# Kernel tuning notes

Hardware: AMD Instinct MI355X
Metric: run time of the kernel (lower is better)

The kernel has to match this reference:

```python
import jax, jax.numpy as jnp
import numpy as np

B, S, IN, H, T, OUT = 128, 336, 64, 1024, 96, 1


def _lstm_step(h, c, x, W_ih, W_hh, b_ih, b_hh):
    # PyTorch LSTM cell: gates in (i, f, g, o) order
    g = x @ W_ih.T + b_ih + h @ W_hh.T + b_hh  # [B, 4H]
    i, f, gg, o = jnp.split(g, 4, axis=-1)
    c_new = jax.nn.sigmoid(f) * c + jax.nn.sigmoid(i) * jnp.tanh(gg)
    h_new = jax.nn.sigmoid(o) * jnp.tanh(c_new)
    return h_new, c_new


def setup_inputs() -> dict:
    key = jax.random.key(0)
    ks = jax.random.split(key, 12)
    s = 0.05
    return {
        "src": jax.random.normal(ks[0], (B, S, IN), jnp.float32),
        "enc_W_ih": jax.random.normal(ks[1], (4 * H, IN), jnp.float32) * s,
        "enc_W_hh": jax.random.normal(ks[2], (4 * H, H), jnp.float32) * s,
        "enc_b_ih": jax.random.normal(ks[3], (4 * H,), jnp.float32) * s,
        "enc_b_hh": jax.random.normal(ks[4], (4 * H,), jnp.float32) * s,
        "dec_W_ih": jax.random.normal(ks[5], (4 * H, OUT + H), jnp.float32) * s,
        "dec_W_hh": jax.random.normal(ks[6], (4 * H, H), jnp.float32) * s,
        "dec_b_ih": jax.random.normal(ks[7], (4 * H,), jnp.float32) * s,
        "dec_b_hh": jax.random.normal(ks[8], (4 * H,), jnp.float32) * s,
        "attn_W": jax.random.normal(ks[9], (H, H), jnp.float32) * s,
        "fc_W": jax.random.normal(ks[10], (OUT, H), jnp.float32) * s,
        "fc_b": jax.random.normal(ks[11], (OUT,), jnp.float32) * s,
        "target_len": T,
    }


def reference(src, enc_W_ih, enc_W_hh, enc_b_ih, enc_b_hh,
              dec_W_ih, dec_W_hh, dec_b_ih, dec_b_hh,
              attn_W, fc_W, fc_b, target_len):
    batch = src.shape[0]
    hdim = enc_W_hh.shape[1]

    # ---- Encoder: single-layer LSTM over src, batch_first ----
    def enc_step(carry, x_t):
        h, c = carry
        h, c = _lstm_step(h, c, x_t, enc_W_ih, enc_W_hh, enc_b_ih, enc_b_hh)
        return (h, c), h

    h0 = jnp.zeros((batch, hdim), src.dtype)
    c0 = jnp.zeros((batch, hdim), src.dtype)
    (h_enc, c_enc), enc_hs = jax.lax.scan(enc_step, (h0, c0),
                                          jnp.swapaxes(src, 0, 1))
    encoder_outputs = jnp.swapaxes(enc_hs, 0, 1)  # [B, S, H]

    def dec_step(carry, _):
        h, c, prev_y = carry
        q = h @ attn_W.T                                      # [B, H]
        energy = jnp.einsum('bh,bsh->bs', q, encoder_outputs)  # [B, S]
        w = jax.nn.softmax(energy, axis=-1)
        ctx = jnp.einsum('bs,bsh->bh', w, encoder_outputs)     # [B, H]
        x = jnp.concatenate([prev_y, ctx], axis=-1)            # [B, OUT+H]
        h, c = _lstm_step(h, c, x, dec_W_ih, dec_W_hh, dec_b_ih, dec_b_hh)
        pred = h @ fc_W.T + fc_b                               # [B, OUT]
        prev_y = jax.lax.stop_gradient(pred)                   # pred.detach()
        return (h, c, prev_y), pred

    prev_y0 = jnp.zeros((batch, fc_W.shape[0]), src.dtype)
    _, preds = jax.lax.scan(dec_step, (h_enc, c_enc, prev_y0), None,
                            length=target_len)
    return jnp.swapaxes(preds, 0, 1)  # [B, target_len, OUT]
```

## Files before the change

### kernel.cpp

```cpp
#include <hip/hip_runtime.h>
#include <math.h>

#define Bn   128
#define Sn   336
#define INd  64
#define Hn   1024
#define Tn   96
#define G4   4096
#define KCE  34
#define KCD  65
#define KCQ  32

typedef __attribute__((ext_vector_type(8))) short short8;
typedef __attribute__((ext_vector_type(4))) float floatx4;
typedef __attribute__((ext_vector_type(4))) unsigned int uintx4;

__device__ __forceinline__ float sigmoidf_(float x){ return 1.0f/(1.0f+expf(-x)); }

__device__ __forceinline__ unsigned short f2bf(float f){
    union { float f; unsigned u; } v; v.f = f;
    unsigned r = v.u + 0x7fffu + ((v.u >> 16) & 1u);
    return (unsigned short)(r >> 16);
}
__device__ __forceinline__ float bflo(unsigned u){ union{unsigned u; float f;} v; v.u = u << 16;        return v.f; }
__device__ __forceinline__ float bfhi(unsigned u){ union{unsigned u; float f;} v; v.u = u & 0xffff0000u; return v.f; }
__device__ __forceinline__ void unpack8v(uintx4 v, float* f){
    f[0]=bflo(v.x); f[1]=bfhi(v.x); f[2]=bflo(v.y); f[3]=bfhi(v.y);
    f[4]=bflo(v.z); f[5]=bfhi(v.z); f[6]=bflo(v.w); f[7]=bfhi(v.w);
}

__global__ void pack_encf(const float* __restrict__ Wih, const float* __restrict__ Whh,
                          const float* __restrict__ bih, const float* __restrict__ bhh,
                          unsigned short* __restrict__ Wp, float* __restrict__ bc){
    long n = (long)256*KCE*512;
    for (long idx = (long)blockIdx.x*256 + threadIdx.x; idx < n; idx += (long)gridDim.x*256){
        int j = (int)(idx & 7), l = (int)((idx >> 3) & 63);
        int kc = (int)((idx >> 9) % KCE);
        int s  = (int)(idx / (KCE*512));
        int c = l & 15, kg = l >> 4;
        int k = kc*32 + kg*8 + j;
        int gate = s & 3, unit = (s >> 2)*16 + c;
        int orig = gate*Hn + unit;
        float v = (k < INd) ? Wih[orig*INd + k] : Whh[(size_t)orig*Hn + (k - INd)];
        Wp[idx] = f2bf(v);
    }
    int tid = blockIdx.x*256 + threadIdx.x;
    if (tid < G4){
        int g = (tid >> 4) & 3, u = (tid >> 6)*16 + (tid & 15);
        int orig = g*Hn + u;
        bc[tid] = bih[orig] + bhh[orig];
    }
}

__global__ void pack_decf(const float* __restrict__ Wih, const float* __restrict__ Whh,
                          const float* __restrict__ bih, const float* __restrict__ bhh,
                          unsigned short* __restrict__ Wp, float* __restrict__ bc){
    long n = (long)256*KCD*512;
    for (long idx = (long)blockIdx.x*256 + threadIdx.x; idx < n; idx += (long)gridDim.x*256){
        int j = (int)(idx & 7), l = (int)((idx >> 3) & 63);
        int kc = (int)((idx >> 9) % KCD);
        int s  = (int)(idx / (KCD*512));
        int c = l & 15, kg = l >> 4;
        int k = kc*32 + kg*8 + j;
        int gate = s & 3, unit = (s >> 2)*16 + c;
        int orig = gate*Hn + unit;
        float v;
        if (k < Hn)          v = Wih[(size_t)orig*(Hn+1) + 1 + k];
        else if (k < 2*Hn)   v = Whh[(size_t)orig*Hn + (k - Hn)];
        else if (k == 2*Hn)  v = Wih[(size_t)orig*(Hn+1)];
        else                 v = 0.0f;
        Wp[idx] = f2bf(v);
    }
    int tid = blockIdx.x*256 + threadIdx.x;
    if (tid < G4){
        int g = (tid >> 4) & 3, u = (tid >> 6)*16 + (tid & 15);
        int orig = g*Hn + u;
        bc[tid] = bih[orig] + bhh[orig];
    }
}

__global__ void pack_attnf(const float* __restrict__ w, unsigned short* __restrict__ Wp){
    int n = 64*KCQ*512;
    for (int idx = blockIdx.x*256 + threadIdx.x; idx < n; idx += gridDim.x*256){
        int j = idx & 7, l = (idx >> 3) & 63;
        int kc = (idx >> 9) & 31;
        int s  = idx >> 14;
        int nn = s*16 + (l & 15);
        int k = kc*32 + (l >> 4)*8 + j;
        Wp[idx] = f2bf(w[(size_t)nn*Hn + k]);
    }
}

__global__ void conv_srcf(const float* __restrict__ s, unsigned short* __restrict__ d){
    int n = Sn*8*2*512;
    for (int idx = blockIdx.x*256 + threadIdx.x; idx < n; idx += gridDim.x*256){
        int j = idx & 7, l = (idx >> 3) & 63;
        int kc = (idx >> 9) & 1, rg = (idx >> 10) & 7, t = idx >> 13;
        int b = rg*16 + (l & 15);
        int k = kc*32 + (l >> 4)*8 + j;
        d[idx] = f2bf(s[((size_t)b*Sn + t)*INd + k]);
    }
}

__global__ void init_ws(unsigned short* __restrict__ hf0, float* __restrict__ cbuf,
                        unsigned short* __restrict__ A0, unsigned short* __restrict__ A1){
    for (int i = blockIdx.x*256 + threadIdx.x; i < 8*KCD*512; i += gridDim.x*256){
        A0[i] = 0; A1[i] = 0;
        if (i < 8*32*512) hf0[i] = 0;
        if (i < Bn*Hn) cbuf[i] = 0.0f;
    }
}

__device__ __forceinline__ void swz(int b, int& x, int& y){
    int xcd = b & 7, li = b >> 3;
    y = xcd*8 + (li & 7);
    x = li >> 3;
}

__global__ __launch_bounds__(256)
void enc_step(const unsigned short* __restrict__ srcfrag,
              const unsigned short* __restrict__ hin,
              const unsigned short* __restrict__ Wf,
              const float* __restrict__ bc, float* __restrict__ cbuf,
              unsigned short* __restrict__ hout,
              unsigned short* __restrict__ enco,
              unsigned short* __restrict__ adec0,
              int t, int last)
{
    __shared__ float red[2][16][65];
    const int tid = threadIdx.x, l = tid & 63, w = tid >> 6;
    const int rgw = w & 1, kh = w >> 1;
    int x, y; swz(blockIdx.x, x, y);
    const int rg = x*2 + rgw;
    const int m0 = rg*16;
    const unsigned short* Bf = Wf + (size_t)(4*y)*KCE*512 + l*8;
    const unsigned short* Ax = srcfrag + ((size_t)t*8 + rg)*2*512 + l*8;
    const unsigned short* Ah = hin + (size_t)rg*32*512 + l*8;
    floatx4 acc0={0,0,0,0}, acc1={0,0,0,0}, acc2={0,0,0,0}, acc3={0,0,0,0};

    if (kh == 0){
        #pragma unroll
        for (int kc = 0; kc < 2; kc++){
            short8 a  = *(const short8*)(Ax + kc*512);
            short8 b0 = *(const short8*)(Bf + (0*KCE + kc)*512);
            short8 b1 = *(const short8*)(Bf + (1*KCE + kc)*512);
            short8 b2 = *(const short8*)(Bf + (2*KCE + kc)*512);
            short8 b3 = *(const short8*)(Bf + (3*KCE + kc)*512);
            acc0 = __builtin_amdgcn_mfma_f32_16x16x32_bf16(a, b0, acc0, 0, 0, 0);
            acc1 = __builtin_amdgcn_mfma_f32_16x16x32_bf16(a, b1, acc1, 0, 0, 0);
            acc2 = __builtin_amdgcn_mfma_f32_16x16x32_bf16(a, b2, acc2, 0, 0, 0);
            acc3 = __builtin_amdgcn_mfma_f32_16x16x32_bf16(a, b3, acc3, 0, 0, 0);
        }
        #pragma unroll 5
        for (int hc = 0; hc < 15; hc++){
            short8 a  = *(const short8*)(Ah + hc*512);
            short8 b0 = *(const short8*)(Bf + (0*KCE + hc + 2)*512);
            short8 b1 = *(const short8*)(Bf + (1*KCE + hc + 2)*512);
            short8 b2 = *(const short8*)(Bf + (2*KCE + hc + 2)*512);
            short8 b3 = *(const short8*)(Bf + (3*KCE + hc + 2)*512);
            acc0 = __builtin_amdgcn_mfma_f32_16x16x32_bf16(a, b0, acc0, 0, 0, 0);
            acc1 = __builtin_amdgcn_mfma_f32_16x16x32_bf16(a, b1, acc1, 0, 0, 0);
            acc2 = __builtin_amdgcn_mfma_f32_16x16x32_bf16(a, b2, acc2, 0, 0, 0);
            acc3 = __builtin_amdgcn_mfma_f32_16x16x32_bf16(a, b3, acc3, 0, 0, 0);
        }
    } else {
        #pragma unroll 5
        for (int hc = 15; hc < 32; hc++){
            short8 a  = *(const short8*)(Ah + hc*512);
            short8 b0 = *(const short8*)(Bf + (0*KCE + hc + 2)*512);
            short8 b1 = *(const short8*)(Bf + (1*KCE + hc + 2)*512);
            short8 b2 = *(const short8*)(Bf + (2*KCE + hc + 2)*512);
            short8 b3 = *(const short8*)(Bf + (3*KCE + hc + 2)*512);
            acc0 = __builtin_amdgcn_mfma_f32_16x16x32_bf16(a, b0, acc0, 0, 0, 0);
            acc1 = __builtin_amdgcn_mfma_f32_16x16x32_bf16(a, b1, acc1, 0, 0, 0);
            acc2 = __builtin_amdgcn_mfma_f32_16x16x32_bf16(a, b2, acc2, 0, 0, 0);
            acc3 = __builtin_amdgcn_mfma_f32_16x16x32_bf16(a, b3, acc3, 0, 0, 0);
        }
        #pragma unroll
        for (int r = 0; r < 4; r++){
            red[rgw][ 0 + r][l] = acc0[r];
            red[rgw][ 4 + r][l] = acc1[r];
            red[rgw][ 8 + r][l] = acc2[r];
            red[rgw][12 + r][l] = acc3[r];
        }
    }
    __syncthreads();
    if (kh != 0) return;
    #pragma unroll
    for (int r = 0; r < 4; r++){
        acc0[r] += red[rgw][ 0 + r][l];
        acc1[r] += red[rgw][ 4 + r][l];
        acc2[r] += red[rgw][ 8 + r][l];
        acc3[r] += red[rgw][12 + r][l];
    }

    const int col = l & 15, q = l >> 4;
    const int u = y*16 + col;
    const float bi  = bc[y*64 + col];
    const float bf_ = bc[y*64 + 16 + col];
    const float bg  = bc[y*64 + 32 + col];
    const float bo  = bc[y*64 + 48 + col];
    const int lsh = ((u >> 3) & 3) * 16;
    #pragma unroll
    for (int r = 0; r < 4; r++){
        const int m = m0 + q*4 + r;
        float gi = acc0[r] + bi;
        float gf = acc1[r] + bf_;
        float gg = acc2[r] + bg;
        float go = acc3[r] + bo;
        float co = cbuf[(size_t)m*Hn + u];
        float cn = sigmoidf_(gf)*co + sigmoidf_(gi)*tanhf(gg);
        float hv = sigmoidf_(go)*tanhf(cn);
        cbuf[(size_t)m*Hn + u] = cn;
        unsigned short hb = f2bf(hv);
        const int lanep = (q*4 + r) + lsh;
        hout[(((size_t)rg*32 + (u >> 5))*64 + lanep)*8 + (u & 7)] = hb;
        __builtin_nontemporal_store(hb, enco + ((size_t)m*Sn + t)*Hn + u);
        if (last) adec0[(((size_t)rg*KCD + 32 + (u >> 5))*64 + lanep)*8 + (u & 7)] = hb;
    }
}

__global__ __launch_bounds__(256)
void dec_step(const unsigned short* __restrict__ Ac,
              const unsigned short* __restrict__ Wf,
              const float* __restrict__ bc, float* __restrict__ cbuf,
              unsigned short* __restrict__ An)
{
    __shared__ float red[2][16][65];
    const int tid = threadIdx.x, l = tid & 63, w = tid >> 6;
    const int rgw = w & 1, kh = w >> 1;
    int x, y; swz(blockIdx.x, x, y);
    const int rg = x*2 + rgw;
    const int m0 = rg*16;
    const unsigned short* Bf = Wf + (size_t)(4*y)*KCD*512 + l*8;
    const unsigned short* Af = Ac + (size_t)rg*KCD*512 + l*8;
    floatx4 acc0={0,0,0,0}, acc1={0,0,0,0}, acc2={0,0,0,0}, acc3={0,0,0,0};

    const int k0 = kh ? 33 : 0;
    const int k1 = kh ? KCD : 33;
    #pragma unroll 5
    for (int kc = k0; kc < k1; kc++){
        short8 a  = *(const short8*)(Af + kc*512);
        short8 b0 = *(const short8*)(Bf + (0*KCD + kc)*512);
        short8 b1 = *(const short8*)(Bf + (1*KCD + kc)*512);
        short8 b2 = *(const short8*)(Bf + (2*KCD + kc)*512);
        short8 b3 = *(const short8*)(Bf + (3*KCD + kc)*512);
        acc0 = __builtin_amdgcn_mfma_f32_16x16x32_bf16(a, b0, acc0, 0, 0, 0);
        acc1 = __builtin_amdgcn_mfma_f32_16x16x32_bf16(a, b1, acc1, 0, 0, 0);
        acc2 = __builtin_amdgcn_mfma_f32_16x16x32_bf16(a, b2, acc2, 0, 0, 0);
        acc3 = __builtin_amdgcn_mfma_f32_16x16x32_bf16(a, b3, acc3, 0, 0, 0);
    }
    if (kh != 0){
        #pragma unroll
        for (int r = 0; r < 4; r++){
            red[rgw][ 0 + r][l] = acc0[r];
            red[rgw][ 4 + r][l] = acc1[r];
            red[rgw][ 8 + r][l] = acc2[r];
            red[rgw][12 + r][l] = acc3[r];
        }
    }
    __syncthreads();
    if (kh != 0) return;
    #pragma unroll
    for (int r = 0; r < 4; r++){
        acc0[r] += red[rgw][ 0 + r][l];
        acc1[r] += red[rgw][ 4 + r][l];
        acc2[r] += red[rgw][ 8 + r][l];
        acc3[r] += red[rgw][12 + r][l];
    }

    const int col = l & 15, q = l >> 4;
    const int u = y*16 + col;
    const float bi  = bc[y*64 + col];
    const float bf_ = bc[y*64 + 16 + col];
    const float bg  = bc[y*64 + 32 + col];
    const float bo  = bc[y*64 + 48 + col];
    const int lsh = ((u >> 3) & 3) * 16;
    #pragma unroll
    for (int r = 0; r < 4; r++){
        const int m = m0 + q*4 + r;
        float gi = acc0[r] + bi;
        float gf = acc1[r] + bf_;
        float gg = acc2[r] + bg;
        float go = acc3[r] + bo;
        float co = cbuf[(size_t)m*Hn + u];
        float cn = sigmoidf_(gf)*co + sigmoidf_(gi)*tanhf(gg);
        float hv = sigmoidf_(go)*tanhf(cn);
        cbuf[(size_t)m*Hn + u] = cn;
        const int lanep = (q*4 + r) + lsh;
        An[(((size_t)rg*KCD + 32 + (u >> 5))*64 + lanep)*8 + (u & 7)] = f2bf(hv);
    }
}

__global__ __launch_bounds__(256)
void attnq_step(const unsigned short* __restrict__ Ac, const unsigned short* __restrict__ Wf,
                unsigned short* __restrict__ qout)
{
    __shared__ float red[2][4][65];
    const int tid = threadIdx.x, l = tid & 63, w = tid >> 6;
    const int rgw = w & 1, kh = w >> 1;
    int x, y; swz(blockIdx.x, x, y);
    const int rg = x*2 + rgw;
    const int m0 = rg*16;
    const unsigned short* Bf = Wf + (size_t)y*KCQ*512 + l*8;
    const unsigned short* Af = Ac + ((size_t)rg*KCD + 32)*512 + l*8;
    floatx4 acc = {0,0,0,0};
    const int k0 = kh ? 16 : 0;
    const int k1 = kh ? 32 : 16;
    #pragma unroll 8
    for (int kc = k0; kc < k1; kc++){
        short8 a = *(const short8*)(Af + kc*512);
        short8 b = *(const short8*)(Bf + kc*512);
        acc = __builtin_amdgcn_mfma_f32_16x16x32_bf16(a, b, acc, 0, 0, 0);
    }
    if (kh != 0){
        #pragma unroll
        for (int r = 0; r < 4; r++) red[rgw][r][l] = acc[r];
    }
    __syncthreads();
    if (kh != 0) return;
    #pragma unroll
    for (int r = 0; r < 4; r++) acc[r] += red[rgw][r][l];

    const int col = l & 15, q = l >> 4;
    #pragma unroll
    for (int r = 0; r < 4; r++){
        const int m = m0 + q*4 + r;
        qout[(size_t)m*Hn + y*16 + col] = f2bf(acc[r]);
    }
}

__global__ __launch_bounds__(512)
void fattn_kernel(const unsigned short* __restrict__ q,
                  const unsigned short* __restrict__ enc,
                  unsigned short* __restrict__ Ac,
                  const float* __restrict__ fcW, const float* __restrict__ fcb,
                  float* __restrict__ out, int d)
{
    __shared__ float ctxl[8*1024];
    __shared__ float mred[8], lred[8];
    __shared__ float fcred[128];
    const int b = blockIdx.x;
    const int tid = threadIdx.x, w = tid >> 6, l = tid & 63;

    float qv[16];
    {
        const uintx4* qp = (const uintx4*)(q + (size_t)b*Hn) + l*2;
        uintx4 q0 = qp[0], q1 = qp[1];
        unpack8v(q0, qv); unpack8v(q1, qv + 8);
    }
    float m = -1e30f, lsum = 0.0f;
    float cacc[16];
    #pragma unroll
    for (int i = 0; i < 16; i++) cacc[i] = 0.0f;

    const uintx4* ebase = (const uintx4*)(enc + (size_t)b*Sn*Hn) + l*2;
    for (int s = w; s < Sn; s += 8){
        uintx4 e0 = __builtin_nontemporal_load(ebase + (size_t)s*128);
        uintx4 e1 = __builtin_nontemporal_load(ebase + (size_t)s*128 + 1);
        float ev[16];
        unpack8v(e0, ev); unpack8v(e1, ev + 8);
        float part = 0.0f;
        #pragma unroll
        for (int i = 0; i < 16; i++) part = fmaf(qv[i], ev[i], part);
        #pragma unroll
        for (int off = 32; off; off >>= 1) part += __shfl_down(part, off);
        float e = __shfl(part, 0);
        float mn = fmaxf(m, e);
        float corr = expf(m - mn);
        float p = expf(e - mn);
        lsum = lsum*corr + p;
        if (corr != 1.0f){
            #pragma unroll
            for (int i = 0; i < 16; i++) cacc[i] *= corr;
        }
        #pragma unroll
        for (int i = 0; i < 16; i++) cacc[i] = fmaf(p, ev[i], cacc[i]);
        m = mn;
    }
    if (l == 0){ mred[w] = m; lred[w] = lsum; }
    __syncthreads();
    float M = mred[0];
    #pragma unroll
    for (int k = 1; k < 8; k++) M = fmaxf(M, mred[k]);
    float corr = expf(m - M);
    #pragma unroll
    for (int j = 0; j < 16; j++) ctxl[w*1024 + j*64 + l] = cacc[j]*corr;
    __syncthreads();
    float L = 0.0f;
    #pragma unroll
    for (int k = 0; k < 8; k++) L += lred[k]*expf(mred[k] - M);
    float invL = 1.0f / L;

    {
        const int u0 = 2*tid;
        float s0 = 0.0f, s1 = 0.0f;
        #pragma unroll
        for (int k = 0; k < 8; k++){
            s0 += ctxl[k*1024 + (u0 & 15)*64 + (u0 >> 4)];
            s1 += ctxl[k*1024 + ((u0+1) & 15)*64 + ((u0+1) >> 4)];
        }
        ushort2 cv; cv.x = f2bf(s0*invL); cv.y = f2bf(s1*invL);
        const int kc = u0 >> 5;
        const int lanep = (b & 15) + ((u0 >> 3) & 3)*16;
        *(ushort2*)(Ac + ((((size_t)(b >> 4))*KCD + kc)*64 + lanep)*8 + (u0 & 7)) = cv;
    }

    float part = 0.0f;
    if (tid < 128){
        const unsigned short* hp = Ac + ((((size_t)(b >> 4))*KCD + 32 + (tid >> 2))*64
                                         + (b & 15) + (tid & 3)*16)*8;
        uintx4 hv = *(const uintx4*)hp;
        float hf[8]; unpack8v(hv, hf);
        #pragma unroll
        for (int j = 0; j < 8; j++) part = fmaf(hf[j], fcW[tid*8 + j], part);
    }
    __syncthreads();
    if (tid < 128) fcred[tid] = part;
    __syncthreads();
    for (int o = 64; o; o >>= 1){
        if (tid < o && tid + o < 128) fcred[tid] += fcred[tid + o];
        __syncthreads();
    }
    if (tid == 0 && d > 0){
        float p = fcred[0] + fcb[0];
        out[b*Tn + (d - 1)] = p;
        Ac[(((size_t)(b >> 4))*KCD + 64)*512 + (b & 15)*8] = f2bf(p);
    }
}

__global__ __launch_bounds__(128)
void fc_final(const unsigned short* __restrict__ A, const float* __restrict__ fcW,
              const float* __restrict__ fcb, float* __restrict__ out){
    __shared__ float red[128];
    const int b = blockIdx.x, tid = threadIdx.x;
    const unsigned short* hp = A + ((((size_t)(b >> 4))*KCD + 32 + (tid >> 2))*64
                                     + (b & 15) + (tid & 3)*16)*8;
    uintx4 hv = *(const uintx4*)hp;
    float hf[8]; unpack8v(hv, hf);
    float part = 0.0f;
    #pragma unroll
    for (int j = 0; j < 8; j++) part = fmaf(hf[j], fcW[tid*8 + j], part);
    red[tid] = part; __syncthreads();
    for (int o = 64; o; o >>= 1){
        if (tid < o) red[tid] += red[tid + o];
        __syncthreads();
    }
    if (tid == 0) out[b*Tn + (Tn - 1)] = red[0] + fcb[0];
}

extern "C" void kernel_launch(void* const* d_in, const int* in_sizes, int n_in,
                              void* d_out, int out_size, void* d_ws, size_t ws_size,
                              hipStream_t stream){
    const float* src  = (const float*)d_in[0];
    const float* eWih = (const float*)d_in[1];
    const float* eWhh = (const float*)d_in[2];
    const float* ebih = (const float*)d_in[3];
    const float* ebhh = (const float*)d_in[4];
    const float* dWih = (const float*)d_in[5];
    const float* dWhh = (const float*)d_in[6];
    const float* dbih = (const float*)d_in[7];
    const float* dbhh = (const float*)d_in[8];
    const float* attnW= (const float*)d_in[9];
    const float* fcW  = (const float*)d_in[10];
    const float* fcb  = (const float*)d_in[11];
    float* out = (float*)d_out;

    char* base = (char*)d_ws;
    auto alloc = [&](size_t bytes){ void* p = base; base += (bytes + 255) & ~255ull; return p; };
    unsigned short* Wencf = (unsigned short*)alloc((size_t)256*KCE*512*2);
    float*          benc  = (float*)alloc(G4*4);
    unsigned short* Wdecf = (unsigned short*)alloc((size_t)256*KCD*512*2);
    float*          bdec  = (float*)alloc(G4*4);
    unsigned short* Wattf = (unsigned short*)alloc((size_t)64*KCQ*512*2);
    unsigned short* srcf  = (unsigned short*)alloc((size_t)Sn*8*2*512*2);
    unsigned short* enco  = (unsigned short*)alloc((size_t)Bn*Sn*Hn*2);
    unsigned short* hf0   = (unsigned short*)alloc((size_t)8*32*512*2);
    unsigned short* hf1   = (unsigned short*)alloc((size_t)8*32*512*2);
    float*          cbuf  = (float*)alloc((size_t)Bn*Hn*4);
    unsigned short* A0f   = (unsigned short*)alloc((size_t)8*KCD*512*2);
    unsigned short* A1f   = (unsigned short*)alloc((size_t)8*KCD*512*2);
    unsigned short* qbf   = (unsigned short*)alloc((size_t)Bn*Hn*2);

    conv_srcf<<<2048, 256, 0, stream>>>(src, srcf);
    pack_encf<<<4096, 256, 0, stream>>>(eWih, eWhh, ebih, ebhh, Wencf, benc);
    pack_decf<<<8192, 256, 0, stream>>>(dWih, dWhh, dbih, dbhh, Wdecf, bdec);
    pack_attnf<<<1024, 256, 0, stream>>>(attnW, Wattf);
    init_ws<<<1040, 256, 0, stream>>>(hf0, cbuf, A0f, A1f);

    unsigned short* hf[2] = {hf0, hf1};
    unsigned short* Ad[2] = {A0f, A1f};

    for (int t = 0; t < Sn; t++){
        enc_step<<<256, 256, 0, stream>>>(srcf, hf[t&1], Wencf, benc, cbuf,
                                          hf[(t+1)&1], enco, A0f, t, t == Sn-1);
    }
    for (int d = 0; d < Tn; d++){
        unsigned short* Ac = Ad[d&1];
        unsigned short* An = Ad[(d+1)&1];
        attnq_step<<<256, 256, 0, stream>>>(Ac, Wattf, qbf);
        fattn_kernel<<<Bn, 512, 0, stream>>>(qbf, enco, Ac, fcW, fcb, out, d);
        dec_step<<<256, 256, 0, stream>>>(Ac, Wdecf, bdec, cbuf, An);
    }
    fc_final<<<Bn, 128, 0, stream>>>(Ad[0], fcW, fcb, out);
}
```

Measured before the change: 9.487 ms.

## Fuse encoder timesteps into one persistent kernel with grid-wide flag barrier

```diff
diff --git a/kernel.cpp b/kernel.cpp
--- a/kernel.cpp
+++ b/kernel.cpp
@@ -103,11 +103,13 @@
 }
 
 __global__ void init_ws(unsigned short* __restrict__ hf0, float* __restrict__ cbuf,
-                        unsigned short* __restrict__ A0, unsigned short* __restrict__ A1){
+                        unsigned short* __restrict__ A0, unsigned short* __restrict__ A1,
+                        unsigned* __restrict__ bar){
     for (int i = blockIdx.x*256 + threadIdx.x; i < 8*KCD*512; i += gridDim.x*256){
         A0[i] = 0; A1[i] = 0;
         if (i < 8*32*512) hf0[i] = 0;
         if (i < Bn*Hn) cbuf[i] = 0.0f;
+        if (i < 256*16 + 16) bar[i] = 0;
     }
 }
 
@@ -117,15 +119,15 @@
     x = li >> 3;
 }
 
-__global__ __launch_bounds__(256)
-void enc_step(const unsigned short* __restrict__ srcfrag,
-              const unsigned short* __restrict__ hin,
-              const unsigned short* __restrict__ Wf,
-              const float* __restrict__ bc, float* __restrict__ cbuf,
-              unsigned short* __restrict__ hout,
-              unsigned short* __restrict__ enco,
-              unsigned short* __restrict__ adec0,
-              int t, int last)
+__global__ __launch_bounds__(256, 1)
+void enc_persist(const unsigned short* __restrict__ srcfrag,
+                 const unsigned short* __restrict__ Wf,
+                 const float* __restrict__ bc, float* __restrict__ cbuf,
+                 unsigned short* __restrict__ h0, unsigned short* __restrict__ h1,
+                 unsigned short* __restrict__ enco,
+                 unsigned short* __restrict__ adec0,
+                 unsigned* __restrict__ flags,
+                 unsigned* __restrict__ go)
 {
     __shared__ float red[2][16][65];
     const int tid = threadIdx.x, l = tid & 63, w = tid >> 6;
@@ -134,66 +136,6 @@
     const int rg = x*2 + rgw;
     const int m0 = rg*16;
     const unsigned short* Bf = Wf + (size_t)(4*y)*KCE*512 + l*8;
-    const unsigned short* Ax = srcfrag + ((size_t)t*8 + rg)*2*512 + l*8;
-    const unsigned short* Ah = hin + (size_t)rg*32*512 + l*8;
-    floatx4 acc0={0,0,0,0}, acc1={0,0,0,0}, acc2={0,0,0,0}, acc3={0,0,0,0};
-
-    if (kh == 0){
-        #pragma unroll
-        for (int kc = 0; kc < 2; kc++){
-            short8 a  = *(const short8*)(Ax + kc*512);
-            short8 b0 = *(const short8*)(Bf + (0*KCE + kc)*512);
-            short8 b1 = *(const short8*)(Bf + (1*KCE + kc)*512);
-            short8 b2 = *(const short8*)(Bf + (2*KCE + kc)*512);
-            short8 b3 = *(const short8*)(Bf + (3*KCE + kc)*512);
-            acc0 = __builtin_amdgcn_mfma_f32_16x16x32_bf16(a, b0, acc0, 0, 0, 0);
-            acc1 = __builtin_amdgcn_mfma_f32_16x16x32_bf16(a, b1, acc1, 0, 0, 0);
-            acc2 = __builtin_amdgcn_mfma_f32_16x16x32_bf16(a, b2, acc2, 0, 0, 0);
-            acc3 = __builtin_amdgcn_mfma_f32_16x16x32_bf16(a, b3, acc3, 0, 0, 0);
-        }
-        #pragma unroll 5
-        for (int hc = 0; hc < 15; hc++){
-            short8 a  = *(const short8*)(Ah + hc*512);
-            short8 b0 = *(const short8*)(Bf + (0*KCE + hc + 2)*512);
-            short8 b1 = *(const short8*)(Bf + (1*KCE + hc + 2)*512);
-            short8 b2 = *(const short8*)(Bf + (2*KCE + hc + 2)*512);
-            short8 b3 = *(const short8*)(Bf + (3*KCE + hc + 2)*512);
-            acc0 = __builtin_amdgcn_mfma_f32_16x16x32_bf16(a, b0, acc0, 0, 0, 0);
-            acc1 = __builtin_amdgcn_mfma_f32_16x16x32_bf16(a, b1, acc1, 0, 0, 0);
-            acc2 = __builtin_amdgcn_mfma_f32_16x16x32_bf16(a, b2, acc2, 0, 0, 0);
-            acc3 = __builtin_amdgcn_mfma_f32_16x16x32_bf16(a, b3, acc3, 0, 0, 0);
-        }
-    } else {
-        #pragma unroll 5
-        for (int hc = 15; hc < 32; hc++){
-            short8 a  = *(const short8*)(Ah + hc*512);
-            short8 b0 = *(const short8*)(Bf + (0*KCE + hc + 2)*512);
-            short8 b1 = *(const short8*)(Bf + (1*KCE + hc + 2)*512);
-            short8 b2 = *(const short8*)(Bf + (2*KCE + hc + 2)*512);
-            short8 b3 = *(const short8*)(Bf + (3*KCE + hc + 2)*512);
-            acc0 = __builtin_amdgcn_mfma_f32_16x16x32_bf16(a, b0, acc0, 0, 0, 0);
-            acc1 = __builtin_amdgcn_mfma_f32_16x16x32_bf16(a, b1, acc1, 0, 0, 0);
-            acc2 = __builtin_amdgcn_mfma_f32_16x16x32_bf16(a, b2, acc2, 0, 0, 0);
-            acc3 = __builtin_amdgcn_mfma_f32_16x16x32_bf16(a, b3, acc3, 0, 0, 0);
-        }
-        #pragma unroll
-        for (int r = 0; r < 4; r++){
-            red[rgw][ 0 + r][l] = acc0[r];
-            red[rgw][ 4 + r][l] = acc1[r];
-            red[rgw][ 8 + r][l] = acc2[r];
-            red[rgw][12 + r][l] = acc3[r];
-        }
-    }
-    __syncthreads();
-    if (kh != 0) return;
-    #pragma unroll
-    for (int r = 0; r < 4; r++){
-        acc0[r] += red[rgw][ 0 + r][l];
-        acc1[r] += red[rgw][ 4 + r][l];
-        acc2[r] += red[rgw][ 8 + r][l];
-        acc3[r] += red[rgw][12 + r][l];
-    }
-
     const int col = l & 15, q = l >> 4;
     const int u = y*16 + col;
     const float bi  = bc[y*64 + col];
@@ -201,22 +143,118 @@
     const float bg  = bc[y*64 + 32 + col];
     const float bo  = bc[y*64 + 48 + col];
     const int lsh = ((u >> 3) & 3) * 16;
-    #pragma unroll
-    for (int r = 0; r < 4; r++){
-        const int m = m0 + q*4 + r;
-        float gi = acc0[r] + bi;
-        float gf = acc1[r] + bf_;
-        float gg = acc2[r] + bg;
-        float go = acc3[r] + bo;
-        float co = cbuf[(size_t)m*Hn + u];
-        float cn = sigmoidf_(gf)*co + sigmoidf_(gi)*tanhf(gg);
-        float hv = sigmoidf_(go)*tanhf(cn);
-        cbuf[(size_t)m*Hn + u] = cn;
-        unsigned short hb = f2bf(hv);
-        const int lanep = (q*4 + r) + lsh;
-        hout[(((size_t)rg*32 + (u >> 5))*64 + lanep)*8 + (u & 7)] = hb;
-        __builtin_nontemporal_store(hb, enco + ((size_t)m*Sn + t)*Hn + u);
-        if (last) adec0[(((size_t)rg*KCD + 32 + (u >> 5))*64 + lanep)*8 + (u & 7)] = hb;
+    float creg[4] = {0,0,0,0};
+    unsigned short* hb[2] = {h0, h1};
+
+    for (int t = 0; t < Sn; t++){
+        const unsigned short* hin = hb[t & 1];
+        unsigned short* hout = hb[(t + 1) & 1];
+        const unsigned short* Ax = srcfrag + ((size_t)t*8 + rg)*2*512 + l*8;
+        const unsigned short* Ah = hin + (size_t)rg*32*512 + l*8;
+        floatx4 acc0={0,0,0,0}, acc1={0,0,0,0}, acc2={0,0,0,0}, acc3={0,0,0,0};
+
+        if (kh == 0){
+            #pragma unroll
+            for (int kc = 0; kc < 2; kc++){
+                short8 a  = *(const short8*)(Ax + kc*512);
+                short8 b0 = *(const short8*)(Bf + (0*KCE + kc)*512);
+                short8 b1 = *(const short8*)(Bf + (1*KCE + kc)*512);
+                short8 b2 = *(const short8*)(Bf + (2*KCE + kc)*512);
+                short8 b3 = *(const short8*)(Bf + (3*KCE + kc)*512);
+                acc0 = __builtin_amdgcn_mfma_f32_16x16x32_bf16(a, b0, acc0, 0, 0, 0);
+                acc1 = __builtin_amdgcn_mfma_f32_16x16x32_bf16(a, b1, acc1, 0, 0, 0);
+                acc2 = __builtin_amdgcn_mfma_f32_16x16x32_bf16(a, b2, acc2, 0, 0, 0);
+                acc3 = __builtin_amdgcn_mfma_f32_16x16x32_bf16(a, b3, acc3, 0, 0, 0);
+            }
+            #pragma unroll 5
+            for (int hc = 0; hc < 15; hc++){
+                short8 a  = *(const short8*)(Ah + hc*512);
+                short8 b0 = *(const short8*)(Bf + (0*KCE + hc + 2)*512);
+                short8 b1 = *(const short8*)(Bf + (1*KCE + hc + 2)*512);
+                short8 b2 = *(const short8*)(Bf + (2*KCE + hc + 2)*512);
+                short8 b3 = *(const short8*)(Bf + (3*KCE + hc + 2)*512);
+                acc0 = __builtin_amdgcn_mfma_f32_16x16x32_bf16(a, b0, acc0, 0, 0, 0);
+                acc1 = __builtin_amdgcn_mfma_f32_16x16x32_bf16(a, b1, acc1, 0, 0, 0);
+                acc2 = __builtin_amdgcn_mfma_f32_16x16x32_bf16(a, b2, acc2, 0, 0, 0);
+                acc3 = __builtin_amdgcn_mfma_f32_16x16x32_bf16(a, b3, acc3, 0, 0, 0);
+            }
+        } else {
+            #pragma unroll 5
+            for (int hc = 15; hc < 32; hc++){
+                short8 a  = *(const short8*)(Ah + hc*512);
+                short8 b0 = *(const short8*)(Bf + (0*KCE + hc + 2)*512);
+                short8 b1 = *(const short8*)(Bf + (1*KCE + hc + 2)*512);
+                short8 b2 = *(const short8*)(Bf + (2*KCE + hc + 2)*512);
+                short8 b3 = *(const short8*)(Bf + (3*KCE + hc + 2)*512);
+                acc0 = __builtin_amdgcn_mfma_f32_16x16x32_bf16(a, b0, acc0, 0, 0, 0);
+                acc1 = __builtin_amdgcn_mfma_f32_16x16x32_bf16(a, b1, acc1, 0, 0, 0);
+                acc2 = __builtin_amdgcn_mfma_f32_16x16x32_bf16(a, b2, acc2, 0, 0, 0);
+                acc3 = __builtin_amdgcn_mfma_f32_16x16x32_bf16(a, b3, acc3, 0, 0, 0);
+            }
+            #pragma unroll
+            for (int r = 0; r < 4; r++){
+                red[rgw][ 0 + r][l] = acc0[r];
+                red[rgw][ 4 + r][l] = acc1[r];
+                red[rgw][ 8 + r][l] = acc2[r];
+                red[rgw][12 + r][l] = acc3[r];
+            }
+        }
+        __syncthreads();
+        if (kh == 0){
+            #pragma unroll
+            for (int r = 0; r < 4; r++){
+                acc0[r] += red[rgw][ 0 + r][l];
+                acc1[r] += red[rgw][ 4 + r][l];
+                acc2[r] += red[rgw][ 8 + r][l];
+                acc3[r] += red[rgw][12 + r][l];
+            }
+            #pragma unroll
+            for (int r = 0; r < 4; r++){
+                const int m = m0 + q*4 + r;
+                float gi = acc0[r] + bi;
+                float gf = acc1[r] + bf_;
+                float gg = acc2[r] + bg;
+                float go_ = acc3[r] + bo;
+                float cn = sigmoidf_(gf)*creg[r] + sigmoidf_(gi)*tanhf(gg);
+                creg[r] = cn;
+                float hv = sigmoidf_(go_)*tanhf(cn);
+                unsigned short hbv = f2bf(hv);
+                const int lanep = (q*4 + r) + lsh;
+                hout[(((size_t)rg*32 + (u >> 5))*64 + lanep)*8 + (u & 7)] = hbv;
+                __builtin_nontemporal_store(hbv, enco + ((size_t)m*Sn + t)*Hn + u);
+                if (t == Sn - 1){
+                    adec0[(((size_t)rg*KCD + 32 + (u >> 5))*64 + lanep)*8 + (u & 7)] = hbv;
+                    cbuf[(size_t)m*Hn + u] = cn;
+                }
+            }
+        }
+        __syncthreads();
+        if (t == Sn - 1) break;
+
+        if (tid == 0)
+            __hip_atomic_store(flags + blockIdx.x*16, (unsigned)(t + 1),
+                               __ATOMIC_RELEASE, __HIP_MEMORY_SCOPE_AGENT);
+        if (blockIdx.x == 0){
+            if (tid < 64){
+                #pragma unroll
+                for (int g = 0; g < 4; g++){
+                    while (__hip_atomic_load(flags + (g*64 + l)*16,
+                                             __ATOMIC_RELAXED, __HIP_MEMORY_SCOPE_AGENT)
+                           < (unsigned)(t + 1))
+                        __builtin_amdgcn_s_sleep(2);
+                }
+            }
+            __syncthreads();
+            if (tid == 0)
+                __hip_atomic_store(go, (unsigned)(t + 1),
+                                   __ATOMIC_RELEASE, __HIP_MEMORY_SCOPE_AGENT);
+        }
+        if (tid == 0){
+            while (__hip_atomic_load(go, __ATOMIC_ACQUIRE, __HIP_MEMORY_SCOPE_AGENT)
+                   < (unsigned)(t + 1))
+                __builtin_amdgcn_s_sleep(2);
+        }
+        __syncthreads();
     }
 }
 
@@ -481,20 +519,19 @@
     unsigned short* A0f   = (unsigned short*)alloc((size_t)8*KCD*512*2);
     unsigned short* A1f   = (unsigned short*)alloc((size_t)8*KCD*512*2);
     unsigned short* qbf   = (unsigned short*)alloc((size_t)Bn*Hn*2);
+    unsigned*       bar   = (unsigned*)alloc((256*16 + 16)*4);
 
     conv_srcf<<<2048, 256, 0, stream>>>(src, srcf);
     pack_encf<<<4096, 256, 0, stream>>>(eWih, eWhh, ebih, ebhh, Wencf, benc);
     pack_decf<<<8192, 256, 0, stream>>>(dWih, dWhh, dbih, dbhh, Wdecf, bdec);
     pack_attnf<<<1024, 256, 0, stream>>>(attnW, Wattf);
-    init_ws<<<1040, 256, 0, stream>>>(hf0, cbuf, A0f, A1f);
-
-    unsigned short* hf[2] = {hf0, hf1};
+    init_ws<<<1040, 256, 0, stream>>>(hf0, cbuf, A0f, A1f, bar);
+
     unsigned short* Ad[2] = {A0f, A1f};
 
-    for (int t = 0; t < Sn; t++){
-        enc_step<<<256, 256, 0, stream>>>(srcf, hf[t&1], Wencf, benc, cbuf,
-                                          hf[(t+1)&1], enco, A0f, t, t == Sn-1);
-    }
+    enc_persist<<<256, 256, 0, stream>>>(srcf, Wencf, benc, cbuf, hf0, hf1,
+                                         enco, A0f, bar, bar + 256*16);
+
     for (int d = 0; d < Tn; d++){
         unsigned short* Ac = Ad[d&1];
         unsigned short* An = Ad[(d+1)&1];
```

After: 16.58 ms. +74.7%, slower.
